# Performance work log

Hardware: AMD Instinct MI355X
Metric: run time of the kernel (lower is better)

## Reference

```python
import jax, jax.numpy as jnp
import numpy as np

NPOINT = 1024
BRANCHES = [(0.4, 32), (0.8, 64)]  # (radius, nsample)
SPECS = [[67, 64, 64, 128], [67, 64, 128, 256]]  # mlp specs after use_xyz (+3)
EPS = 1e-5


def setup_inputs() -> dict:
    key = jax.random.key(0)
    ks = jax.random.split(key, 16)
    B, N, C = 8, 8192, 64
    inp = {
        "xyz": jax.random.normal(ks[0], (B, N, 3), jnp.float32),
        "features": jax.random.normal(ks[1], (B, C, N), jnp.float32),
    }
    ki = 2
    for bi, spec in enumerate(SPECS):
        for li in range(3):
            o, i = spec[li + 1], spec[li]
            inp[f"w{bi}_{li}"] = jax.random.normal(ks[ki], (o, i), jnp.float32) * (1.0 / np.sqrt(i)); ki += 1
            inp[f"g{bi}_{li}"] = jnp.ones((o,), jnp.float32)
            inp[f"b{bi}_{li}"] = jnp.zeros((o,), jnp.float32)
    return inp


def fps(pts, npoint):
    # pts: [B, N+1, 3] (mean point prepended); sequential farthest point sampling
    B, N1, _ = pts.shape

    def step(carry, _):
        dist, far = carry
        idx3 = jnp.broadcast_to(far[:, None, None], (B, 1, 3))
        centroid = jnp.take_along_axis(pts, idx3, axis=1)  # [B,1,3]
        d = jnp.sum((pts - centroid) ** 2, axis=-1)        # [B,N+1]
        dist = jnp.minimum(dist, d)
        far2 = jnp.argmax(dist, axis=-1)
        return (dist, far2), centroid[:, 0, :]

    dist0 = jnp.full((B, N1), 1e10, jnp.float32)
    far0 = jnp.zeros((B,), jnp.int32)
    _, locs = jax.lax.scan(step, (dist0, far0), None, length=npoint)
    return jnp.transpose(locs, (1, 0, 2))  # [B, npoint, 3]


def ball_query(xyz, new_xyz, radius, nsample):
    # first <=nsample indices with dist^2 < radius^2, padded with first valid (0 if none)
    B, N, _ = xyz.shape
    d2 = jnp.sum((new_xyz[:, :, None, :] - xyz[:, None, :, :]) ** 2, axis=-1)  # [B,S,N]
    score = jnp.where(d2 < radius * radius, jnp.arange(N, dtype=jnp.int32), N)
    vals, _ = jax.lax.top_k(-score, nsample)  # smallest scores = earliest valid indices
    idx = -vals                               # [B,S,nsample], N marks invalid
    first = idx[..., :1]
    first = jnp.where(first < N, first, 0)
    return jnp.where(idx < N, idx, first)


def _forward(xyz, features, params):
    mean = jnp.mean(xyz, axis=1, keepdims=True)
    pts = jnp.concatenate([mean, xyz], axis=1)          # prepend mean point
    new_xyz = jax.lax.stop_gradient(fps(pts, NPOINT))   # [B,npoint,3] (torch no_grad)
    outs = []
    for (radius, nsample), layers in zip(BRANCHES, params):
        idx = ball_query(xyz, new_xyz, radius, nsample)           # [B,S,K]
        gxyz = jax.vmap(lambda p, i: p[i])(xyz, idx)              # [B,S,K,3]
        rel = jnp.transpose(gxyz - new_xyz[:, :, None, :], (0, 3, 1, 2))  # [B,3,S,K]
        gfeat = jax.vmap(lambda f, i: f[:, i])(features, idx)     # [B,C,S,K]
        x = jnp.concatenate([rel, gfeat], axis=1)                 # [B,3+C,S,K]
        for W, g, b in layers:  # Conv2d 1x1 (no bias) + BatchNorm (train stats) + ReLU
            x = jnp.einsum('oi,bisk->bosk', W, x)
            m = jnp.mean(x, axis=(0, 2, 3), keepdims=True)
            v = jnp.var(x, axis=(0, 2, 3), keepdims=True)
            x = (x - m) / jnp.sqrt(v + EPS) * g[None, :, None, None] + b[None, :, None, None]
            x = jax.nn.relu(x)
        outs.append(jnp.max(x, axis=3))                           # [B,Cout,S]
    return new_xyz, jnp.concatenate(outs, axis=1)


def reference(xyz, features,
              w0_0, g0_0, b0_0, w0_1, g0_1, b0_1, w0_2, g0_2, b0_2,
              w1_0, g1_0, b1_0, w1_1, g1_1, b1_1, w1_2, g1_2, b1_2):
    params = [
        [(w0_0, g0_0, b0_0), (w0_1, g0_1, b0_1), (w0_2, g0_2, b0_2)],
        [(w1_0, g1_0, b1_0), (w1_1, g1_1, b1_1), (w1_2, g1_2, b1_2)],
    ]
    return _forward(xyz, features, params)
```

## Files before the change

### kernel.cpp

```cpp
#include <hip/hip_runtime.h>
#include <hip/hip_bf16.h>
#include <cstdint>


typedef __attribute__((ext_vector_type(8))) short short8;
typedef __attribute__((ext_vector_type(4))) float f32x4;
typedef __attribute__((ext_vector_type(2))) float f32x2;

__device__ __forceinline__ float bf2f(unsigned short u) {
    return __uint_as_float(((unsigned)u) << 16);
}
__device__ __forceinline__ unsigned short f2bf(float f) {
    unsigned u = __float_as_uint(f);
    return (unsigned short)((u + 0x7fffu + ((u >> 16) & 1u)) >> 16);
}

__device__ __forceinline__ float wave_red_max_f32(float v) {
#define DPPSTEP(ctrl)                                                                  \
    {                                                                                  \
        int _t = __builtin_amdgcn_update_dpp((int)0xFF800000, __float_as_int(v), ctrl, \
                                             0xf, 0xf, false);                         \
        v = fmaxf(v, __int_as_float(_t));                                              \
    }
    DPPSTEP(0x111) DPPSTEP(0x112) DPPSTEP(0x114) DPPSTEP(0x118) DPPSTEP(0x142) DPPSTEP(0x143)
#undef DPPSTEP
    return v;
}
__device__ __forceinline__ unsigned wave_red_min_u32(unsigned v) {
#define DPPSTEP(ctrl)                                                                   \
    {                                                                                   \
        unsigned _t = (unsigned)__builtin_amdgcn_update_dpp((int)0xFFFFFFFF, (int)v,    \
                                                            ctrl, 0xf, 0xf, false);     \
        v = v < _t ? v : _t;                                                            \
    }
    DPPSTEP(0x111) DPPSTEP(0x112) DPPSTEP(0x114) DPPSTEP(0x118) DPPSTEP(0x142) DPPSTEP(0x143)
#undef DPPSTEP
    return v;
}
__device__ __forceinline__ unsigned long long u64max(unsigned long long a, unsigned long long b) {
    return a > b ? a : b;
}
__device__ __forceinline__ unsigned u32min(unsigned a, unsigned b) { return a < b ? a : b; }

static const size_t OFF_WBF   = 0;
static const size_t OFF_STATS = 262144;
static const size_t STATS_BYTES = 720896;
static const size_t OFF_AFF   = 1048576;
static const size_t OFF_IDX0  = 2097152;
static const size_t OFF_IDX1  = 3145728;
static const size_t OFF_MX    = 5242880;
static const size_t OFF_MN    = 13631488;
static const size_t OFF_Y0    = 22020096;
static const size_t OFF_Y1    = 90177536;
static const size_t OFF_FEATT = 211812352;

__global__ __launch_bounds__(256) void fused_pre(
    const float* __restrict__ xyz, const float* __restrict__ feat,
    float* __restrict__ newxyz, unsigned short* __restrict__ ft,
    const float* __restrict__ w0, const float* __restrict__ w1, const float* __restrict__ w2,
    const float* __restrict__ w3, const float* __restrict__ w4, const float* __restrict__ w5,
    unsigned short* __restrict__ wb) {
    __shared__ union alignas(16) SM {
        struct {
            float ptsx[8200], ptsy[8200], ptsz[8200];
            float ldsM[16][3];
            float meanv[3];
            alignas(16) unsigned long long sKey[2][4];
            float cbuf[3072];
        } f;
        float tile[64][65];
    } sm;
    const int tid = threadIdx.x;

    if (blockIdx.x >= 1032) {
        int id = (int)(blockIdx.x - 1032) * 256 + tid;
        const int psz[6] = {6144, 4096, 8192, 6144, 8192, 32768};
        const int Kp[6] = {96, 64, 64, 96, 64, 128};
        const int Ks[6] = {67, 64, 64, 67, 64, 128};
        const float* wp[6] = {w0, w1, w2, w3, w4, w5};
        int off = 0;
        for (int l = 0; l < 6; ++l) {
            if (id < off + psz[l]) {
                int e = id - off;
                int m = e / Kp[l], k = e - m * Kp[l];
                float v = (k < Ks[l]) ? wp[l][m * Ks[l] + k] : 0.f;
                wb[id] = f2bf(v);
                return;
            }
            off += psz[l];
        }
        return;
    }

    if (blockIdx.x >= 8) {
        int tb = (int)blockIdx.x - 8;
        int b = tb >> 7;
        int j0 = (tb & 127) * 64;
#pragma unroll
        for (int i = 0; i < 16; ++i) {
            int e = i * 256 + tid;
            int c = e >> 6, j = e & 63;
            sm.tile[j][c] = feat[((size_t)b * 64 + c) * 8192 + j0 + j];
        }
        __syncthreads();
#pragma unroll
        for (int i = 0; i < 16; ++i) {
            int e = i * 256 + tid;
            int j = e >> 6, c = e & 63;
            ft[((size_t)(b * 8192 + j0 + j)) * 96 + 3 + c] = f2bf(sm.tile[j][c]);
        }
        if (tid < 64) {
            int j = tid;
            size_t base = ((size_t)(b * 8192 + j0 + j)) * 96;
            const float* xp = xyz + ((size_t)b * 8192 + j0 + j) * 3;
            ft[base + 0] = f2bf(xp[0]);
            ft[base + 1] = f2bf(xp[1]);
            ft[base + 2] = f2bf(xp[2]);
        } else if (tid < 128) {
            int j = tid - 64;
            size_t base = ((size_t)(b * 8192 + j0 + j)) * 96;
            for (int c = 67; c < 96; ++c) ft[base + c] = 0;
        }
        return;
    }

    const int b = blockIdx.x;
    const int t = tid;
    const int lane = t & 63, wv = t >> 6;
    const float* xb = xyz + (size_t)b * 8192 * 3;

    f32x2 px[16], py[16], pz[16], d[16];
#pragma unroll
    for (int k = 0; k < 16; ++k) {
        int q0 = t + 256 * (2 * k);
        int q1 = t + 256 * (2 * k + 1);
        px[k].x = xb[q0 * 3 + 0]; px[k].y = xb[q1 * 3 + 0];
        py[k].x = xb[q0 * 3 + 1]; py[k].y = xb[q1 * 3 + 1];
        pz[k].x = xb[q0 * 3 + 2]; pz[k].y = xb[q1 * 3 + 2];
        d[k].x = 1e10f; d[k].y = 1e10f;
        sm.f.ptsx[q0 + 1] = px[k].x; sm.f.ptsx[q1 + 1] = px[k].y;
        sm.f.ptsy[q0 + 1] = py[k].x; sm.f.ptsy[q1 + 1] = py[k].y;
        sm.f.ptsz[q0 + 1] = pz[k].x; sm.f.ptsz[q1 + 1] = pz[k].y;
    }
    {
        float sx[4], sy[4], sz[4];
#pragma unroll
        for (int m = 0; m < 4; ++m) {
            int u = (t + 256 * m + 1023) & 1023;
            float ax = 0.f, ay = 0.f, az = 0.f;
#pragma unroll
            for (int jj = 0; jj < 8; ++jj) {
                int ia = u + 1024 * jj;
                ax += xb[ia * 3 + 0]; ay += xb[ia * 3 + 1]; az += xb[ia * 3 + 2];
            }
            sx[m] = ax; sy[m] = ay; sz[m] = az;
        }
#pragma unroll
        for (int off = 32; off; off >>= 1) {
#pragma unroll
            for (int m = 0; m < 4; ++m) {
                sx[m] += __shfl_xor(sx[m], off, 64);
                sy[m] += __shfl_xor(sy[m], off, 64);
                sz[m] += __shfl_xor(sz[m], off, 64);
            }
        }
        if (lane == 0) {
#pragma unroll
            for (int m = 0; m < 4; ++m) {
                sm.f.ldsM[wv + 4 * m][0] = sx[m];
                sm.f.ldsM[wv + 4 * m][1] = sy[m];
                sm.f.ldsM[wv + 4 * m][2] = sz[m];
            }
        }
    }
    __syncthreads();
    if (t < 3) {
        float s = 0.f;
        for (int w = 0; w < 16; ++w) s += sm.f.ldsM[w][t];
        sm.f.meanv[t] = s * (1.f / 8192.f);
    }
    __syncthreads();
    float cx = sm.f.meanv[0], cy = sm.f.meanv[1], cz = sm.f.meanv[2];
    const float mmx = cx, mmy = cy, mmz = cz;
    float dm = 1e10f;
    if (t == 0) { sm.f.ptsx[0] = cx; sm.f.ptsy[0] = cy; sm.f.ptsz[0] = cz; }
    __syncthreads();

    for (int it = 0; it < 1024; ++it) {
        if (t == 0) {
            sm.f.cbuf[it * 3 + 0] = cx;
            sm.f.cbuf[it * 3 + 1] = cy;
            sm.f.cbuf[it * 3 + 2] = cz;
        }
        f32x2 c0, c1, c2;
        c0.x = cx; c0.y = cx; c1.x = cy; c1.y = cy; c2.x = cz; c2.y = cz;
        float bv = -1e30f;
        unsigned bi = 0u;
        {
#pragma clang fp contract(off)
#pragma unroll
            for (int k = 0; k < 16; ++k) {
                f32x2 dx = px[k] - c0;
                f32x2 dy = py[k] - c1;
                f32x2 dz = pz[k] - c2;
                f32x2 dd = (dx * dx + dy * dy) + dz * dz;
                f32x2 nd = __builtin_elementwise_min(d[k], dd);
                d[k] = nd;
                bool g0 = nd.x > bv;
                bv = fmaxf(bv, nd.x);
                bi = g0 ? (unsigned)(t + 256 * (2 * k) + 1) : bi;
                bool g1 = nd.y > bv;
                bv = fmaxf(bv, nd.y);
                bi = g1 ? (unsigned)(t + 256 * (2 * k + 1) + 1) : bi;
            }
        }
        if (t == 0) {
            float dx = __fsub_rn(mmx, cx);
            float dy = __fsub_rn(mmy, cy);
            float dz = __fsub_rn(mmz, cz);
            float dd = __fadd_rn(__fadd_rn(__fmul_rn(dx, dx), __fmul_rn(dy, dy)), __fmul_rn(dz, dz));
            dm = fminf(dm, dd);
            bv = fmaxf(bv, dm);
        }
        float wm = wave_red_max_f32(bv);
        float bmaxw = __int_as_float(__builtin_amdgcn_readlane(__float_as_int(wm), 63));
        unsigned mi = (bv == bmaxw) ? bi : 0xFFFFFFFFu;
        if (t == 0 && dm == bmaxw) mi = 0u;
        unsigned wmin = wave_red_min_u32(mi);
        unsigned miw = (unsigned)__builtin_amdgcn_readlane((int)wmin, 63);
        int par = it & 1;
        if (lane == 0)
            sm.f.sKey[par][wv] = ((unsigned long long)__float_as_uint(bmaxw) << 32) |
                                 (unsigned long long)(8192u - miw);
        __syncthreads();
        ulonglong2 kp0 = *(const ulonglong2*)&sm.f.sKey[par][0];
        ulonglong2 kp1 = *(const ulonglong2*)&sm.f.sKey[par][2];
        unsigned long long kk = u64max(u64max(kp0.x, kp0.y), u64max(kp1.x, kp1.y));
        int far = 8192 - (int)(unsigned)(kk & 0xffffffffull);
        cx = sm.f.ptsx[far];
        cy = sm.f.ptsy[far];
        cz = sm.f.ptsz[far];
    }
    __syncthreads();
    float* ob = newxyz + (size_t)b * 3072;
#pragma unroll
    for (int i = 0; i < 12; ++i) ob[t + 256 * i] = sm.f.cbuf[t + 256 * i];
}

__global__ void ball_query2(const float* __restrict__ xyz, const float* __restrict__ newxyz,
                            int* __restrict__ idx0, int* __restrict__ idx1) {
    int bid = blockIdx.x;
    int br = (bid >= 2048);
    int K = br ? 64 : 32;
    float r2 = br ? (0.8f * 0.8f) : (0.4f * 0.4f);
    int* idxout = br ? idx1 : idx0;
    int wid = (((bid & 2047) * 256) + threadIdx.x) >> 6;
    int lane = threadIdx.x & 63;
    int b = wid >> 10;
    const float* q = newxyz + (size_t)wid * 3;
    float qx = q[0], qy = q[1], qz = q[2];
    const float* xb = xyz + (size_t)b * 8192 * 3;
    int* out = idxout + (size_t)wid * K;
    int count = 0;
    int first = 0;
    for (int base = 0; base < 8192 && count < K; base += 64) {
        int j = base + lane;
        float dx = __fsub_rn(xb[j * 3 + 0], qx);
        float dy = __fsub_rn(xb[j * 3 + 1], qy);
        float dz = __fsub_rn(xb[j * 3 + 2], qz);
        float d2 = __fadd_rn(__fadd_rn(__fmul_rn(dx, dx), __fmul_rn(dy, dy)), __fmul_rn(dz, dz));
        bool in = d2 < r2;
        unsigned long long m = __ballot(in);
        if (count == 0 && m) first = base + __ffsll((long long)m) - 1;
        if (in) {
            int pos = count + __popcll(m & ((1ull << lane) - 1ull));
            if (pos < K) out[pos] = j;
        }
        count += __popcll(m);
    }
    if (count < K) {
        int fillv = (count > 0) ? first : 0;
        for (int p = count + lane; p < K; p += 64) out[p] = fillv;
    }
}

template <int Mp, int Kp, int KSH, int NT>
__global__ __launch_bounds__(256) void gemm_gather(
    const unsigned short* __restrict__ Wb, const int* __restrict__ idx,
    const unsigned short* __restrict__ ftp, const float* __restrict__ newxyz,
    unsigned short* __restrict__ Yout, float* __restrict__ statS, float* __restrict__ statQ) {
    constexpr int MT = Mp / 64;
    constexpr int KS = Kp / 32;
    constexpr int NC = NT * 16;
    constexpr int NCHUNK = NT * KS * 64;
    __shared__ unsigned short Bs[NCHUNK * 8];
    __shared__ float sAux[NT * 64];
    int* sAuxI = (int*)sAux;

    const int tid = threadIdx.x;
    const int w = tid >> 6;
    const int lane = tid & 63;
    const int n = lane & 15;
    const int quad = lane >> 4;
    const int rbase = w * (Mp / 4);
    const long col0 = (long)blockIdx.x * NC;

    short8 a[MT][KS];
#pragma unroll
    for (int mt = 0; mt < MT; ++mt)
#pragma unroll
        for (int ks = 0; ks < KS; ++ks)
            a[mt][ks] = *(const short8*)(Wb + (size_t)(rbase + mt * 16 + n) * Kp + ks * 32 + quad * 8);

    for (int c = tid; c < NC; c += 256) {
        long colg = col0 + c;
        sAuxI[c] = idx[colg];
        long sk = colg >> KSH;
        sAux[NC + c] = newxyz[sk * 3 + 0];
        sAux[2 * NC + c] = newxyz[sk * 3 + 1];
        sAux[3 * NC + c] = newxyz[sk * 3 + 2];
    }
    __syncthreads();

#pragma unroll
    for (int i = 0; i < NCHUNK / 256; ++i) {
        int p = i * 256 + tid;
        int pl = p & 63;
        int pn = pl & 15;
        int pq = pl >> 4;
        int rest = p >> 6;
        int pks = rest % KS;
        int pnt = rest / KS;
        int col = pnt * 16 + pn;
        int kc = pks * 4 + pq;
        const int bb = (int)(col0 >> (KSH + 10));
        int j = sAuxI[col];
        short8 v = *(const short8*)(ftp + ((long)(bb * 8192 + j)) * 96 + kc * 8);
        if (kc == 0) {
            v[0] = (short)f2bf(bf2f((unsigned short)v[0]) - sAux[NC + col]);
            v[1] = (short)f2bf(bf2f((unsigned short)v[1]) - sAux[2 * NC + col]);
            v[2] = (short)f2bf(bf2f((unsigned short)v[2]) - sAux[3 * NC + col]);
        }
        *(short8*)(&Bs[p * 8]) = v;
    }
    __syncthreads();

    f32x4 acc[MT][NT];
#pragma unroll
    for (int mt = 0; mt < MT; ++mt)
#pragma unroll
        for (int nt = 0; nt < NT; ++nt)
#pragma unroll
            for (int r = 0; r < 4; ++r) acc[mt][nt][r] = 0.f;

#pragma unroll
    for (int ks = 0; ks < KS; ++ks) {
#pragma unroll
        for (int nt = 0; nt < NT; ++nt) {
            short8 bfr = *(const short8*)(&Bs[((nt * KS + ks) * 64 + lane) * 8]);
#pragma unroll
            for (int mt = 0; mt < MT; ++mt)
                acc[mt][nt] = __builtin_amdgcn_mfma_f32_16x16x32_bf16(a[mt][ks], bfr, acc[mt][nt], 0, 0, 0);
        }
    }

    const int slot = (int)(blockIdx.x & 127);
#pragma unroll
    for (int mt = 0; mt < MT; ++mt)
#pragma unroll
        for (int r = 0; r < 4; ++r) {
            float s = 0.f, q = 0.f;
#pragma unroll
            for (int nt = 0; nt < NT; ++nt) {
                float v = acc[mt][nt][r];
                s += v;
                q = fmaf(v, v, q);
            }
#pragma unroll
            for (int off = 1; off < 16; off <<= 1) {
                s += __shfl_xor(s, off, 16);
                q += __shfl_xor(q, off, 16);
            }
            if (n == 0) {
                int ch = rbase + mt * 16 + quad * 4 + r;
                atomicAdd(statS + (size_t)ch * 128 + slot, s);
                atomicAdd(statQ + (size_t)ch * 128 + slot, q);
            }
        }

#pragma unroll
    for (int mt = 0; mt < MT; ++mt)
#pragma unroll
        for (int nt = 0; nt < NT; ++nt) {
            long col = col0 + nt * 16 + n;
            unsigned p0 = f2bf(acc[mt][nt][0]) | ((unsigned)f2bf(acc[mt][nt][1]) << 16);
            unsigned p1 = f2bf(acc[mt][nt][2]) | ((unsigned)f2bf(acc[mt][nt][3]) << 16);
            uint2 st; st.x = p0; st.y = p1;
            *(uint2*)(Yout + col * Mp + rbase + mt * 16 + quad * 4) = st;
        }
}

#define STAGE_IN1(TILE, BUFI)                                                       \
    {                                                                               \
        long scol0 = (long)(TILE) * NC;                                             \
        short8 raw[CPT];                                                            \
        _Pragma("unroll") for (int i = 0; i < CPT; ++i)                             \
            raw[i] = *(const short8*)(Xin + (scol0 + colC[i]) * (long)Kp + kcC[i] * 8); \
        _Pragma("unroll") for (int i = 0; i < CPT; ++i) {                           \
            short8 v;                                                               \
            _Pragma("unroll") for (int e = 0; e < 8; ++e) {                         \
                float xf = bf2f((unsigned short)raw[i][e]);                         \
                xf = fmaxf(fmaf(xf, sAff[kcC[i] * 8 + e], sAff[Kp + kcC[i] * 8 + e]), 0.f); \
                v[e] = (short)f2bf(xf);                                             \
            }                                                                       \
            *(short8*)(&Bs[(BUFI)][(i * 256 + tid) * 8]) = v;                       \
        }                                                                           \
    }

template <int Mp, int Kp, int OUT_MODE, int KSH, int NT>
__global__ __launch_bounds__(256) void gemm_pers(
    const unsigned short* __restrict__ Wb, const unsigned short* __restrict__ Xin,
    const float* __restrict__ aff, unsigned short* __restrict__ Yout,
    float* __restrict__ MX, float* __restrict__ MN,
    float* __restrict__ statS, float* __restrict__ statQ, int ntiles) {
    constexpr int MT = Mp / 64;
    constexpr int KS = Kp / 32;
    constexpr int NC = NT * 16;
    constexpr int NCHUNK = NT * KS * 64;
    constexpr int CPT = NCHUNK / 256;
    __shared__ unsigned short Bs[2][NCHUNK * 8];
    __shared__ float sAff[2 * 128];

    const int tid = threadIdx.x;
    const int w = tid >> 6;
    const int lane = tid & 63;
    const int n = lane & 15;
    const int quad = lane >> 4;
    const int rbase = w * (Mp / 4);

    int colC[CPT], kcC[CPT];
    {
        int pl = tid & 63;
        int pn = pl & 15;
        int pq = pl >> 4;
#pragma unroll
        for (int i = 0; i < CPT; ++i) {
            int rest = i * 4 + (tid >> 6);
            int pks = rest % KS;
            int pnt = rest / KS;
            colC[i] = pnt * 16 + pn;
            kcC[i] = pks * 4 + pq;
        }
    }

    short8 a[MT][KS];
#pragma unroll
    for (int mt = 0; mt < MT; ++mt)
#pragma unroll
        for (int ks = 0; ks < KS; ++ks)
            a[mt][ks] = *(const short8*)(Wb + (size_t)(rbase + mt * 16 + n) * Kp + ks * 32 + quad * 8);

    if (tid < 2 * Kp) sAff[tid] = aff[tid];
    float accS[MT][4], accQ[MT][4];
#pragma unroll
    for (int mt = 0; mt < MT; ++mt)
#pragma unroll
        for (int r = 0; r < 4; ++r) { accS[mt][r] = 0.f; accQ[mt][r] = 0.f; }
    __syncthreads();

    if ((int)blockIdx.x < ntiles) STAGE_IN1((int)blockIdx.x, 0);
    __syncthreads();

    int g = 0;
    for (int t = (int)blockIdx.x; t < ntiles; t += (int)gridDim.x, ++g) {
        int tn = t + (int)gridDim.x;
        if (tn < ntiles) STAGE_IN1(tn, (g + 1) & 1);

        const int cur = g & 1;
        const long col0 = (long)t * NC;
        f32x4 acc[MT][NT];
#pragma unroll
        for (int mt = 0; mt < MT; ++mt)
#pragma unroll
            for (int nt = 0; nt < NT; ++nt)
#pragma unroll
                for (int r = 0; r < 4; ++r) acc[mt][nt][r] = 0.f;

#pragma unroll
        for (int ks = 0; ks < KS; ++ks) {
#pragma unroll
            for (int nt = 0; nt < NT; ++nt) {
                short8 bfr = *(const short8*)(&Bs[cur][((nt * KS + ks) * 64 + lane) * 8]);
#pragma unroll
                for (int mt = 0; mt < MT; ++mt)
                    acc[mt][nt] =
                        __builtin_amdgcn_mfma_f32_16x16x32_bf16(a[mt][ks], bfr, acc[mt][nt], 0, 0, 0);
            }
        }

#pragma unroll
        for (int mt = 0; mt < MT; ++mt)
#pragma unroll
            for (int r = 0; r < 4; ++r) {
                float s = accS[mt][r], q = accQ[mt][r];
#pragma unroll
                for (int nt = 0; nt < NT; ++nt) {
                    float v = acc[mt][nt][r];
                    s += v;
                    q = fmaf(v, v, q);
                }
                accS[mt][r] = s;
                accQ[mt][r] = q;
            }

        if constexpr (OUT_MODE == 0) {
#pragma unroll
            for (int mt = 0; mt < MT; ++mt)
#pragma unroll
                for (int nt = 0; nt < NT; ++nt) {
                    long col = col0 + nt * 16 + n;
                    unsigned p0 = f2bf(acc[mt][nt][0]) | ((unsigned)f2bf(acc[mt][nt][1]) << 16);
                    unsigned p1 = f2bf(acc[mt][nt][2]) | ((unsigned)f2bf(acc[mt][nt][3]) << 16);
                    uint2 st; st.x = p0; st.y = p1;
                    *(uint2*)(Yout + col * Mp + rbase + mt * 16 + quad * 4) = st;
                }
        } else {
            constexpr int GRP = (1 << KSH) / 16;
            constexpr int NG = NT / GRP;
#pragma unroll
            for (int mt = 0; mt < MT; ++mt)
#pragma unroll
                for (int r = 0; r < 4; ++r) {
#pragma unroll
                    for (int gh = 0; gh < NG; ++gh) {
                        float mx = acc[mt][GRP * gh][r], mn = acc[mt][GRP * gh][r];
#pragma unroll
                        for (int e = 1; e < GRP; ++e) {
                            mx = fmaxf(mx, acc[mt][GRP * gh + e][r]);
                            mn = fminf(mn, acc[mt][GRP * gh + e][r]);
                        }
#pragma unroll
                        for (int off = 1; off < 16; off <<= 1) {
                            mx = fmaxf(mx, __shfl_xor(mx, off, 16));
                            mn = fminf(mn, __shfl_xor(mn, off, 16));
                        }
                        if (n == 0) {
                            int ch = rbase + mt * 16 + quad * 4 + r;
                            long gg = (col0 >> KSH) + gh;
                            MX[(long)ch * 8192 + gg] = mx;
                            MN[(long)ch * 8192 + gg] = mn;
                        }
                    }
                }
        }
        __syncthreads();
    }

    const int slot = (int)(blockIdx.x & 127);
#pragma unroll
    for (int mt = 0; mt < MT; ++mt)
#pragma unroll
        for (int r = 0; r < 4; ++r) {
            float s = accS[mt][r], q = accQ[mt][r];
#pragma unroll
            for (int off = 1; off < 16; off <<= 1) {
                s += __shfl_xor(s, off, 16);
                q += __shfl_xor(q, off, 16);
            }
            if (n == 0) {
                int ch = rbase + mt * 16 + quad * 4 + r;
                atomicAdd(statS + (size_t)ch * 128 + slot, s);
                atomicAdd(statQ + (size_t)ch * 128 + slot, q);
            }
        }
}

__global__ void finalize_kernel(const float* __restrict__ sS, const float* __restrict__ sQ,
                                const float* __restrict__ g, const float* __restrict__ b,
                                float* __restrict__ aff, int C, float invCount) {
    int c = threadIdx.x + blockIdx.x * blockDim.x;
    if (c >= C) return;
    float s = 0.f, q = 0.f;
    for (int k = 0; k < 128; ++k) { s += sS[c * 128 + k]; q += sQ[c * 128 + k]; }
    float mean = s * invCount;
    float var = fmaxf(q * invCount - mean * mean, 0.f);
    float sc = g[c] / sqrtf(var + 1e-5f);
    float sh = b[c] - mean * sc;
    aff[c] = sc;
    aff[C + c] = sh;
}

__global__ void final_out_kernel(const float* __restrict__ MX, const float* __restrict__ MN,
                                 const float* __restrict__ aff, float* __restrict__ out1,
                                 int Cout, int cOff) {
    long i = (long)blockIdx.x * 256 + threadIdx.x;
    int c = (int)(i >> 13);
    int gidx = (int)(i & 8191);
    int b = gidx >> 10, s = gidx & 1023;
    float sc = aff[c], sh = aff[Cout + c];
    float v = fmaxf(fmaxf(sc * MX[i] + sh, sc * MN[i] + sh), 0.f);
    out1[((long)b * 384 + cOff + c) * 1024 + s] = v;
}

extern "C" void kernel_launch(void* const* d_in, const int* in_sizes, int n_in,
                              void* d_out, int out_size, void* d_ws, size_t ws_size,
                              hipStream_t stream) {
    const float* xyz = (const float*)d_in[0];
    const float* feat = (const float*)d_in[1];
    const float *W[6], *G[6], *Bi[6];
    for (int l = 0; l < 6; ++l) {
        W[l] = (const float*)d_in[2 + l * 3];
        G[l] = (const float*)d_in[3 + l * 3];
        Bi[l] = (const float*)d_in[4 + l * 3];
    }
    char* ws = (char*)d_ws;
    float* out0 = (float*)d_out;
    float* out1 = (float*)d_out + 24576;

    unsigned short* wb = (unsigned short*)(ws + OFF_WBF);
    float* stats = (float*)(ws + OFF_STATS);
    float* affine = (float*)(ws + OFF_AFF);
    int* idx0 = (int*)(ws + OFF_IDX0);
    int* idx1 = (int*)(ws + OFF_IDX1);
    float* mx = (float*)(ws + OFF_MX);
    float* mn = (float*)(ws + OFF_MN);
    unsigned short* y0 = (unsigned short*)(ws + OFF_Y0);
    unsigned short* y1 = (unsigned short*)(ws + OFF_Y1);
    unsigned short* ftp = (unsigned short*)(ws + OFF_FEATT);

    hipMemsetAsync(stats, 0, STATS_BYTES, stream);
    fused_pre<<<1288, 256, 0, stream>>>(xyz, feat, out0, ftp, W[0], W[1], W[2], W[3], W[4],
                                        W[5], wb);
    ball_query2<<<4096, 256, 0, stream>>>(xyz, out0, idx0, idx1);

    const int wOff[6] = {0, 6144, 10240, 18432, 24576, 32768};
    int stOff[6], afOff[6];
    {
        const int Cs[6] = {64, 64, 128, 64, 128, 256};
        int so = 0, ao = 0;
        for (int l = 0; l < 6; ++l) {
            stOff[l] = so; so += Cs[l] * 256;
            afOff[l] = ao; ao += Cs[l] * 2;
        }
    }
    const float ic0 = 1.f / (float)(8L * 1024 * 32);
    const float ic1 = 1.f / (float)(8L * 1024 * 64);
    const int GRID = 768;

    gemm_gather<64, 96, 5, 16><<<1024, 256, 0, stream>>>(
        wb + wOff[0], idx0, ftp, out0, y0, stats + stOff[0], stats + stOff[0] + 64 * 128);
    finalize_kernel<<<1, 256, 0, stream>>>(stats + stOff[0], stats + stOff[0] + 64 * 128,
                                           G[0], Bi[0], affine + afOff[0], 64, ic0);
    gemm_pers<64, 64, 0, 5, 8><<<GRID, 256, 0, stream>>>(
        wb + wOff[1], y0, affine + afOff[0], y1, nullptr, nullptr, stats + stOff[1],
        stats + stOff[1] + 64 * 128, 2048);
    finalize_kernel<<<1, 256, 0, stream>>>(stats + stOff[1], stats + stOff[1] + 64 * 128,
                                           G[1], Bi[1], affine + afOff[1], 64, ic0);
    gemm_pers<128, 64, 1, 5, 8><<<GRID, 256, 0, stream>>>(
        wb + wOff[2], y1, affine + afOff[1], nullptr, mx, mn, stats + stOff[2],
        stats + stOff[2] + 128 * 128, 2048);
    finalize_kernel<<<1, 256, 0, stream>>>(stats + stOff[2], stats + stOff[2] + 128 * 128,
                                           G[2], Bi[2], affine + afOff[2], 128, ic0);
    final_out_kernel<<<(128 * 8192) / 256, 256, 0, stream>>>(mx, mn, affine + afOff[2], out1,
                                                             128, 0);

    gemm_gather<64, 96, 6, 16><<<2048, 256, 0, stream>>>(
        wb + wOff[3], idx1, ftp, out0, y0, stats + stOff[3], stats + stOff[3] + 64 * 128);
    finalize_kernel<<<1, 256, 0, stream>>>(stats + stOff[3], stats + stOff[3] + 64 * 128,
                                           G[3], Bi[3], affine + afOff[3], 64, ic1);
    gemm_pers<128, 64, 0, 6, 8><<<GRID, 256, 0, stream>>>(
        wb + wOff[4], y0, affine + afOff[3], y1, nullptr, nullptr, stats + stOff[4],
        stats + stOff[4] + 128 * 128, 4096);
    finalize_kernel<<<1, 256, 0, stream>>>(stats + stOff[4], stats + stOff[4] + 128 * 128,
                                           G[4], Bi[4], affine + afOff[4], 128, ic1);
    gemm_pers<256, 128, 1, 6, 4><<<GRID, 256, 0, stream>>>(
        wb + wOff[5], y1, affine + afOff[4], nullptr, mx, mn, stats + stOff[5],
        stats + stOff[5] + 256 * 128, 8192);
    finalize_kernel<<<1, 256, 0, stream>>>(stats + stOff[5], stats + stOff[5] + 256 * 128,
                                           G[5], Bi[5], affine + afOff[5], 256, ic1);
    final_out_kernel<<<(256 * 8192) / 256, 256, 0, stream>>>(mx, mn, affine + afOff[5], out1,
                                                             256, 128);
}
```

Before: 1.523 ms.

## Make gather GEMM persistent with double-buffered gathers and fold BN finalize into consumers

Converts the first-layer gather GEMM into a persistent kernel over a fixed grid. It double-buffers the gathered feature tile and the index/centroid auxiliary data, so the next tile's gather overlaps the current MFMA work, and it accumulates per-channel stats in registers across tiles before a single atomic flush. It also removes four single-block finalize launches by having each consumer gemm_pers reduce the previous layer's partial sums and compute the BN scale and shift in its prologue. The cost is redundant stat reduction in every block and extra LDS from double buffering.

```diff
diff --git a/kernel.cpp b/kernel.cpp
--- a/kernel.cpp
+++ b/kernel.cpp
@@ -285,17 +285,18 @@
 }
 
 template <int Mp, int Kp, int KSH, int NT>
-__global__ __launch_bounds__(256) void gemm_gather(
+__global__ __launch_bounds__(256) void gemm_gather_pers(
     const unsigned short* __restrict__ Wb, const int* __restrict__ idx,
     const unsigned short* __restrict__ ftp, const float* __restrict__ newxyz,
-    unsigned short* __restrict__ Yout, float* __restrict__ statS, float* __restrict__ statQ) {
+    unsigned short* __restrict__ Yout, float* __restrict__ statS, float* __restrict__ statQ,
+    int ntiles) {
     constexpr int MT = Mp / 64;
     constexpr int KS = Kp / 32;
     constexpr int NC = NT * 16;
     constexpr int NCHUNK = NT * KS * 64;
-    __shared__ unsigned short Bs[NCHUNK * 8];
-    __shared__ float sAux[NT * 64];
-    int* sAuxI = (int*)sAux;
+    constexpr int CPT = NCHUNK / 256;
+    __shared__ unsigned short Bs[2][NCHUNK * 8];
+    __shared__ float sAuxF[2][NC * 4];
 
     const int tid = threadIdx.x;
     const int w = tid >> 6;
@@ -303,7 +304,22 @@
     const int n = lane & 15;
     const int quad = lane >> 4;
     const int rbase = w * (Mp / 4);
-    const long col0 = (long)blockIdx.x * NC;
+    const int G = (int)gridDim.x;
+
+    int colC[CPT], kcC[CPT];
+    {
+        int pl = tid & 63;
+        int pn = pl & 15;
+        int pq = pl >> 4;
+#pragma unroll
+        for (int i = 0; i < CPT; ++i) {
+            int rest = i * 4 + (tid >> 6);
+            int pks = rest % KS;
+            int pnt = rest / KS;
+            colC[i] = pnt * 16 + pn;
+            kcC[i] = pks * 4 + pq;
+        }
+    }
 
     short8 a[MT][KS];
 #pragma unroll
@@ -312,70 +328,115 @@
         for (int ks = 0; ks < KS; ++ks)
             a[mt][ks] = *(const short8*)(Wb + (size_t)(rbase + mt * 16 + n) * Kp + ks * 32 + quad * 8);
 
-    for (int c = tid; c < NC; c += 256) {
-        long colg = col0 + c;
-        sAuxI[c] = idx[colg];
-        long sk = colg >> KSH;
-        sAux[NC + c] = newxyz[sk * 3 + 0];
-        sAux[2 * NC + c] = newxyz[sk * 3 + 1];
-        sAux[3 * NC + c] = newxyz[sk * 3 + 2];
-    }
+    float accS[MT][4], accQ[MT][4];
+#pragma unroll
+    for (int mt = 0; mt < MT; ++mt)
+#pragma unroll
+        for (int r = 0; r < 4; ++r) { accS[mt][r] = 0.f; accQ[mt][r] = 0.f; }
+
+#define STAGE_AUX(TILE, AUXI)                                   \
+    {                                                           \
+        long scol0 = (long)(TILE) * NC;                         \
+        if (tid < NC) {                                         \
+            long colg = scol0 + tid;                            \
+            ((int*)&sAuxF[(AUXI)][0])[tid] = idx[colg];         \
+            long sk = colg >> KSH;                              \
+            sAuxF[(AUXI)][NC + tid] = newxyz[sk * 3 + 0];       \
+            sAuxF[(AUXI)][2 * NC + tid] = newxyz[sk * 3 + 1];   \
+            sAuxF[(AUXI)][3 * NC + tid] = newxyz[sk * 3 + 2];   \
+        }                                                       \
+    }
+
+#define STAGE_GATHER(TILE, BUFI, AUXI)                                                   \
+    {                                                                                    \
+        long scol0 = (long)(TILE) * NC;                                                  \
+        const int bb = (int)(scol0 >> (KSH + 10));                                       \
+        int jj[CPT];                                                                     \
+        _Pragma("unroll") for (int i = 0; i < CPT; ++i)                                  \
+            jj[i] = ((const int*)&sAuxF[(AUXI)][0])[colC[i]];                            \
+        short8 raw[CPT];                                                                 \
+        _Pragma("unroll") for (int i = 0; i < CPT; ++i)                                  \
+            raw[i] = *(const short8*)(ftp + ((long)(bb * 8192 + jj[i])) * 96 + kcC[i] * 8); \
+        _Pragma("unroll") for (int i = 0; i < CPT; ++i) {                                \
+            short8 v = raw[i];                                                           \
+            if (kcC[i] == 0) {                                                           \
+                v[0] = (short)f2bf(bf2f((unsigned short)v[0]) - sAuxF[(AUXI)][NC + colC[i]]); \
+                v[1] = (short)f2bf(bf2f((unsigned short)v[1]) - sAuxF[(AUXI)][2 * NC + colC[i]]); \
+                v[2] = (short)f2bf(bf2f((unsigned short)v[2]) - sAuxF[(AUXI)][3 * NC + colC[i]]); \
+            }                                                                            \
+            *(short8*)(&Bs[(BUFI)][(i * 256 + tid) * 8]) = v;                            \
+        }                                                                                \
+    }
+
+    const int t0 = (int)blockIdx.x;
+    STAGE_AUX(t0, 0)
     __syncthreads();
-
-#pragma unroll
-    for (int i = 0; i < NCHUNK / 256; ++i) {
-        int p = i * 256 + tid;
-        int pl = p & 63;
-        int pn = pl & 15;
-        int pq = pl >> 4;
-        int rest = p >> 6;
-        int pks = rest % KS;
-        int pnt = rest / KS;
-        int col = pnt * 16 + pn;
-        int kc = pks * 4 + pq;
-        const int bb = (int)(col0 >> (KSH + 10));
-        int j = sAuxI[col];
-        short8 v = *(const short8*)(ftp + ((long)(bb * 8192 + j)) * 96 + kc * 8);
-        if (kc == 0) {
-            v[0] = (short)f2bf(bf2f((unsigned short)v[0]) - sAux[NC + col]);
-            v[1] = (short)f2bf(bf2f((unsigned short)v[1]) - sAux[2 * NC + col]);
-            v[2] = (short)f2bf(bf2f((unsigned short)v[2]) - sAux[3 * NC + col]);
-        }
-        *(short8*)(&Bs[p * 8]) = v;
-    }
+    STAGE_GATHER(t0, 0, 0)
+    if (t0 + G < ntiles) STAGE_AUX(t0 + G, 1)
     __syncthreads();
 
-    f32x4 acc[MT][NT];
+    int g = 0;
+    for (int t = t0; t < ntiles; t += G, ++g) {
+        const int cur = g & 1;
+        const int nxt = cur ^ 1;
+        if (t + G < ntiles) STAGE_GATHER(t + G, nxt, nxt)
+        if (t + 2 * G < ntiles) STAGE_AUX(t + 2 * G, cur)
+
+        const long col0 = (long)t * NC;
+        f32x4 acc[MT][NT];
+#pragma unroll
+        for (int mt = 0; mt < MT; ++mt)
+#pragma unroll
+            for (int nt = 0; nt < NT; ++nt)
+#pragma unroll
+                for (int r = 0; r < 4; ++r) acc[mt][nt][r] = 0.f;
+
+#pragma unroll
+        for (int ks = 0; ks < KS; ++ks) {
+#pragma unroll
+            for (int nt = 0; nt < NT; ++nt) {
+                short8 bfr = *(const short8*)(&Bs[cur][((nt * KS + ks) * 64 + lane) * 8]);
+#pragma unroll
+                for (int mt = 0; mt < MT; ++mt)
+                    acc[mt][nt] =
+                        __builtin_amdgcn_mfma_f32_16x16x32_bf16(a[mt][ks], bfr, acc[mt][nt], 0, 0, 0);
+            }
+        }
+
+#pragma unroll
+        for (int mt = 0; mt < MT; ++mt)
+#pragma unroll
+            for (int r = 0; r < 4; ++r) {
+                float s = accS[mt][r], q = accQ[mt][r];
+#pragma unroll
+                for (int nt = 0; nt < NT; ++nt) {
+                    float v = acc[mt][nt][r];
+                    s += v;
+                    q = fmaf(v, v, q);
+                }
+                accS[mt][r] = s;
+                accQ[mt][r] = q;
+            }
+
+#pragma unroll
+        for (int mt = 0; mt < MT; ++mt)
+#pragma unroll
+            for (int nt = 0; nt < NT; ++nt) {
+                long col = col0 + nt * 16 + n;
+                unsigned p0 = f2bf(acc[mt][nt][0]) | ((unsigned)f2bf(acc[mt][nt][1]) << 16);
+                unsigned p1 = f2bf(acc[mt][nt][2]) | ((unsigned)f2bf(acc[mt][nt][3]) << 16);
+                uint2 st; st.x = p0; st.y = p1;
+                *(uint2*)(Yout + col * Mp + rbase + mt * 16 + quad * 4) = st;
+            }
+        __syncthreads();
+    }
+
+    const int slot = (int)(blockIdx.x & 127);
 #pragma unroll
     for (int mt = 0; mt < MT; ++mt)
 #pragma unroll
-        for (int nt = 0; nt < NT; ++nt)
-#pragma unroll
-            for (int r = 0; r < 4; ++r) acc[mt][nt][r] = 0.f;
-
-#pragma unroll
-    for (int ks = 0; ks < KS; ++ks) {
-#pragma unroll
-        for (int nt = 0; nt < NT; ++nt) {
-            short8 bfr = *(const short8*)(&Bs[((nt * KS + ks) * 64 + lane) * 8]);
-#pragma unroll
-            for (int mt = 0; mt < MT; ++mt)
-                acc[mt][nt] = __builtin_amdgcn_mfma_f32_16x16x32_bf16(a[mt][ks], bfr, acc[mt][nt], 0, 0, 0);
-        }
-    }
-
-    const int slot = (int)(blockIdx.x & 127);
-#pragma unroll
-    for (int mt = 0; mt < MT; ++mt)
-#pragma unroll
         for (int r = 0; r < 4; ++r) {
-            float s = 0.f, q = 0.f;
-#pragma unroll
-            for (int nt = 0; nt < NT; ++nt) {
-                float v = acc[mt][nt][r];
-                s += v;
-                q = fmaf(v, v, q);
-            }
+            float s = accS[mt][r], q = accQ[mt][r];
 #pragma unroll
             for (int off = 1; off < 16; off <<= 1) {
                 s += __shfl_xor(s, off, 16);
@@ -387,17 +448,8 @@
                 atomicAdd(statQ + (size_t)ch * 128 + slot, q);
             }
         }
-
-#pragma unroll
-    for (int mt = 0; mt < MT; ++mt)
-#pragma unroll
-        for (int nt = 0; nt < NT; ++nt) {
-            long col = col0 + nt * 16 + n;
-            unsigned p0 = f2bf(acc[mt][nt][0]) | ((unsigned)f2bf(acc[mt][nt][1]) << 16);
-            unsigned p1 = f2bf(acc[mt][nt][2]) | ((unsigned)f2bf(acc[mt][nt][3]) << 16);
-            uint2 st; st.x = p0; st.y = p1;
-            *(uint2*)(Yout + col * Mp + rbase + mt * 16 + quad * 4) = st;
-        }
+#undef STAGE_AUX
+#undef STAGE_GATHER
 }
 
 #define STAGE_IN1(TILE, BUFI)                                                       \
@@ -420,8 +472,9 @@
 template <int Mp, int Kp, int OUT_MODE, int KSH, int NT>
 __global__ __launch_bounds__(256) void gemm_pers(
     const unsigned short* __restrict__ Wb, const unsigned short* __restrict__ Xin,
-    const float* __restrict__ aff, unsigned short* __restrict__ Yout,
-    float* __restrict__ MX, float* __restrict__ MN,
+    const float* __restrict__ pS, const float* __restrict__ pQ,
+    const float* __restrict__ gW, const float* __restrict__ bW, float invC,
+    unsigned short* __restrict__ Yout, float* __restrict__ MX, float* __restrict__ MN,
     float* __restrict__ statS, float* __restrict__ statQ, int ntiles) {
     constexpr int MT = Mp / 64;
     constexpr int KS = Kp / 32;
@@ -460,7 +513,24 @@
         for (int ks = 0; ks < KS; ++ks)
             a[mt][ks] = *(const short8*)(Wb + (size_t)(rbase + mt * 16 + n) * Kp + ks * 32 + quad * 8);
 
-    if (tid < 2 * Kp) sAff[tid] = aff[tid];
+    if (tid < Kp) {
+        const f32x4* s4 = (const f32x4*)(pS + (size_t)tid * 128);
+        const f32x4* q4 = (const f32x4*)(pQ + (size_t)tid * 128);
+        float s = 0.f, q = 0.f;
+#pragma unroll 4
+        for (int k = 0; k < 32; ++k) {
+            f32x4 vs = s4[k];
+            f32x4 vq = q4[k];
+            s += vs.x; s += vs.y; s += vs.z; s += vs.w;
+            q += vq.x; q += vq.y; q += vq.z; q += vq.w;
+        }
+        float mean = s * invC;
+        float var = fmaxf(q * invC - mean * mean, 0.f);
+        float sc = gW[tid] / sqrtf(var + 1e-5f);
+        float sh = bW[tid] - mean * sc;
+        sAff[tid] = sc;
+        sAff[Kp + tid] = sh;
+    }
     float accS[MT][4], accQ[MT][4];
 #pragma unroll
     for (int mt = 0; mt < MT; ++mt)
@@ -647,35 +717,27 @@
     const float ic1 = 1.f / (float)(8L * 1024 * 64);
     const int GRID = 768;
 
-    gemm_gather<64, 96, 5, 16><<<1024, 256, 0, stream>>>(
-        wb + wOff[0], idx0, ftp, out0, y0, stats + stOff[0], stats + stOff[0] + 64 * 128);
-    finalize_kernel<<<1, 256, 0, stream>>>(stats + stOff[0], stats + stOff[0] + 64 * 128,
-                                           G[0], Bi[0], affine + afOff[0], 64, ic0);
+    gemm_gather_pers<64, 96, 5, 8><<<GRID, 256, 0, stream>>>(
+        wb + wOff[0], idx0, ftp, out0, y0, stats + stOff[0], stats + stOff[0] + 64 * 128, 2048);
     gemm_pers<64, 64, 0, 5, 8><<<GRID, 256, 0, stream>>>(
-        wb + wOff[1], y0, affine + afOff[0], y1, nullptr, nullptr, stats + stOff[1],
-        stats + stOff[1] + 64 * 128, 2048);
-    finalize_kernel<<<1, 256, 0, stream>>>(stats + stOff[1], stats + stOff[1] + 64 * 128,
-                                           G[1], Bi[1], affine + afOff[1], 64, ic0);
+        wb + wOff[1], y0, stats + stOff[0], stats + stOff[0] + 64 * 128, G[0], Bi[0], ic0, y1,
+        nullptr, nullptr, stats + stOff[1], stats + stOff[1] + 64 * 128, 2048);
     gemm_pers<128, 64, 1, 5, 8><<<GRID, 256, 0, stream>>>(
-        wb + wOff[2], y1, affine + afOff[1], nullptr, mx, mn, stats + stOff[2],
-        stats + stOff[2] + 128 * 128, 2048);
+        wb + wOff[2], y1, stats + stOff[1], stats + stOff[1] + 64 * 128, G[1], Bi[1], ic0,
+        nullptr, mx, mn, stats + stOff[2], stats + stOff[2] + 128 * 128, 2048);
     finalize_kernel<<<1, 256, 0, stream>>>(stats + stOff[2], stats + stOff[2] + 128 * 128,
                                            G[2], Bi[2], affine + afOff[2], 128, ic0);
     final_out_kernel<<<(128 * 8192) / 256, 256, 0, stream>>>(mx, mn, affine + afOff[2], out1,
                                                              128, 0);
 
-    gemm_gather<64, 96, 6, 16><<<2048, 256, 0, stream>>>(
-        wb + wOff[3], idx1, ftp, out0, y0, stats + stOff[3], stats + stOff[3] + 64 * 128);
-    finalize_kernel<<<1, 256, 0, stream>>>(stats + stOff[3], stats + stOff[3] + 64 * 128,
-                                           G[3], Bi[3], affine + afOff[3], 64, ic1);
+    gemm_gather_pers<64, 96, 6, 8><<<GRID, 256, 0, stream>>>(
+        wb + wOff[3], idx1, ftp, out0, y0, stats + stOff[3], stats + stOff[3] + 64 * 128, 4096);
     gemm_pers<128, 64, 0, 6, 8><<<GRID, 256, 0, stream>>>(
-        wb + wOff[4], y0, affine + afOff[3], y1, nullptr, nullptr, stats + stOff[4],
-        stats + stOff[4] + 128 * 128, 4096);
-    finalize_kernel<<<1, 256, 0, stream>>>(stats + stOff[4], stats + stOff[4] + 128 * 128,
-                                           G[4], Bi[4], affine + afOff[4], 128, ic1);
+        wb + wOff[4], y0, stats + stOff[3], stats + stOff[3] + 64 * 128, G[3], Bi[3], ic1, y1,
+        nullptr, nullptr, stats + stOff[4], stats + stOff[4] + 128 * 128, 4096);
     gemm_pers<256, 128, 1, 6, 4><<<GRID, 256, 0, stream>>>(
-        wb + wOff[5], y1, affine + afOff[4], nullptr, mx, mn, stats + stOff[5],
-        stats + stOff[5] + 256 * 128, 8192);
+        wb + wOff[5], y1, stats + stOff[4], stats + stOff[4] + 128 * 128, G[4], Bi[4], ic1,
+        nullptr, mx, mn, stats + stOff[5], stats + stOff[5] + 256 * 128, 8192);
     finalize_kernel<<<1, 256, 0, stream>>>(stats + stOff[5], stats + stOff[5] + 256 * 128,
                                            G[5], Bi[5], affine + afOff[5], 256, ic1);
     final_out_kernel<<<(256 * 8192) / 256, 256, 0, stream>>>(mx, mn, affine + afOff[5], out1,
```

New measurement: 1.516 ms. Within noise of the previous version (-0.5%).
